# Optimization experiments

Hardware: AMD Instinct MI355X
Metric: run time of the kernel (lower is better)

## Reference

```python
import jax, jax.numpy as jnp
import numpy as np

B, T, N, P = 64, 288, 1024, 12


def setup_inputs() -> dict:
    key = jax.random.key(0)
    k1, k2 = jax.random.split(key)
    x = jax.random.normal(k1, (B, T, N, 1), dtype=jnp.float32)
    # scale AR coefficients so the self-feeding recurrence stays numerically stable
    ar_params = jax.random.normal(k2, (N, P), dtype=jnp.float32) * 0.05
    bias = jnp.zeros((N,), dtype=jnp.float32)
    return {"x": x, "ar_params": ar_params, "bias": bias}


def reference(x, ar_params, bias):
    # x: (B, T, N, 1); ar_params: (N, p); bias: (N,)
    Bd, Td, Nd, _ = x.shape
    p = ar_params.shape[1]
    # initial history window = last p entries of the full input series per (b, n)
    h0 = jnp.transpose(x[:, Td - p:, :, 0], (0, 2, 1))  # (B, N, p)

    def step(h, _):
        # per-node AR(p): dot of node coefficients with its rolling history
        pred = jnp.einsum('np,bnp->bn', ar_params, h) + bias  # (B, N)
        h = jnp.concatenate([h[:, :, 1:], pred[:, :, None]], axis=-1)
        return h, pred

    _, preds = jax.lax.scan(step, h0, None, length=Td)  # (T, B, N)
    return jnp.transpose(preds, (1, 0, 2))[..., None]  # (B, T, N, 1)
```

## Files before the change

kernel.cpp:

```cpp
#include <hip/hip_runtime.h>


constexpr int B = 64;
constexpr int T = 288;
constexpr int N = 1024;
constexpr int P = 12;
constexpr int CHUNK = 72;
constexpr int NCHUNK = T / CHUNK;

__global__ __launch_bounds__(256) void ar_chunked_kernel(
    const float* __restrict__ x,
    const float* __restrict__ ar,
    const float* __restrict__ bias,
    float* __restrict__ out)
{
    const int tid = blockIdx.x * blockDim.x + threadIdx.x;
    const int n = tid & (N - 1);
    const int b = (tid >> 10) & (B - 1);
    const int c = tid >> 16;

    float a[P];
    const float* arow = ar + n * P;
#pragma unroll
    for (int j = 0; j < P; ++j) a[j] = arow[j];
    const float bs = bias[n];

    float acc[P];
#pragma unroll
    for (int s = 0; s < P; ++s) acc[s] = bs;

    const float* xb = x + (size_t)b * T * N + (size_t)(T - P) * N + n;
#pragma unroll
    for (int i = 0; i < P; ++i) {
        const float hv = xb[(size_t)i * N];
#pragma unroll
        for (int t = 0; t <= i; ++t)
            acc[t] = fmaf(a[i - t], hv, acc[t]);
    }

    const int skip = c * CHUNK;
#pragma unroll 1
    for (int tt = 0; tt < skip; tt += P) {
#pragma unroll
        for (int k = 0; k < P; ++k) {
            const float pred = acc[k];
            acc[k] = fmaf(a[0], pred, bs);
#pragma unroll
            for (int d = 1; d < P; ++d)
                acc[(k + d) % P] = fmaf(a[P - d], pred, acc[(k + d) % P]);
        }
    }

    float* ob = out + (size_t)b * T * N + (size_t)skip * N + n;
#pragma unroll 1
    for (int tt = 0; tt < CHUNK; tt += P) {
#pragma unroll
        for (int k = 0; k < P; ++k) {
            const float pred = acc[k];
            ob[(size_t)(tt + k) * N] = pred;
            acc[k] = fmaf(a[0], pred, bs);
#pragma unroll
            for (int d = 1; d < P; ++d)
                acc[(k + d) % P] = fmaf(a[P - d], pred, acc[(k + d) % P]);
        }
    }
}

extern "C" void kernel_launch(void* const* d_in, const int* in_sizes, int n_in,
                              void* d_out, int out_size, void* d_ws, size_t ws_size,
                              hipStream_t stream) {
    const float* x    = (const float*)d_in[0];
    const float* ar   = (const float*)d_in[1];
    const float* bias = (const float*)d_in[2];
    float* out = (float*)d_out;

    const int total = B * N * NCHUNK;
    ar_chunked_kernel<<<total / 256, 256, 0, stream>>>(x, ar, bias, out);
}
```

Baseline: 126.4 us.

## Process four nodes per thread with float4 loads and stores

Each thread now runs the AR recurrence for four adjacent nodes, loading coefficients, bias, history and writing outputs as float4. The grid shrinks to one block per (batch, chunk) and the chunk count stays at four. This aims to cut memory instruction count and add instruction-level parallelism across independent recurrences. In exchange it raises register pressure and leaves far fewer waves per CU to hide latency.

```diff
diff --git a/kernel.cpp b/kernel.cpp
--- a/kernel.cpp
+++ b/kernel.cpp
@@ -5,64 +5,74 @@
 constexpr int T = 288;
 constexpr int N = 1024;
 constexpr int P = 12;
-constexpr int CHUNK = 72;
-constexpr int NCHUNK = T / CHUNK;
+constexpr int G = 4;
+constexpr int NCHUNK = 4;
+constexpr int CHUNK = T / NCHUNK;
 
-__global__ __launch_bounds__(256) void ar_chunked_kernel(
+#define STEP12(STORE_EXPR)                                                     \
+  _Pragma("unroll") for (int k = 0; k < P; ++k) {                              \
+    float pr[G];                                                               \
+    _Pragma("unroll") for (int g = 0; g < G; ++g) {                            \
+      const float pred = acc[g][k];                                            \
+      pr[g] = pred;                                                            \
+      acc[g][k] = fmaf(a[g][0], pred, bs[g]);                                  \
+      _Pragma("unroll") for (int d = 1; d < P; ++d)                            \
+        acc[g][(k + d) % P] = fmaf(a[g][P - d], pred, acc[g][(k + d) % P]);    \
+    }                                                                          \
+    STORE_EXPR;                                                                \
+  }
+
+__global__ __launch_bounds__(256) void ar_vec4_kernel(
     const float* __restrict__ x,
     const float* __restrict__ ar,
     const float* __restrict__ bias,
     float* __restrict__ out)
 {
-    const int tid = blockIdx.x * blockDim.x + threadIdx.x;
-    const int n = tid & (N - 1);
-    const int b = (tid >> 10) & (B - 1);
-    const int c = tid >> 16;
+    const int b = blockIdx.x & (B - 1);
+    const int c = blockIdx.x >> 6;
+    const int n0 = threadIdx.x * G;
 
-    float a[P];
-    const float* arow = ar + n * P;
+    float a[G][P];
 #pragma unroll
-    for (int j = 0; j < P; ++j) a[j] = arow[j];
-    const float bs = bias[n];
+    for (int g = 0; g < G; ++g) {
+        const float4* ap = (const float4*)(ar + (size_t)(n0 + g) * P);
+        const float4 a0 = ap[0], a1 = ap[1], a2 = ap[2];
+        a[g][0] = a0.x; a[g][1] = a0.y; a[g][2]  = a0.z; a[g][3]  = a0.w;
+        a[g][4] = a1.x; a[g][5] = a1.y; a[g][6]  = a1.z; a[g][7]  = a1.w;
+        a[g][8] = a2.x; a[g][9] = a2.y; a[g][10] = a2.z; a[g][11] = a2.w;
+    }
+    const float4 bv = *(const float4*)(bias + n0);
+    const float bs[G] = {bv.x, bv.y, bv.z, bv.w};
 
-    float acc[P];
+    float acc[G][P];
 #pragma unroll
-    for (int s = 0; s < P; ++s) acc[s] = bs;
+    for (int g = 0; g < G; ++g)
+#pragma unroll
+        for (int s = 0; s < P; ++s) acc[g][s] = bs[g];
 
-    const float* xb = x + (size_t)b * T * N + (size_t)(T - P) * N + n;
+    const float* xb = x + ((size_t)b * T + (T - P)) * N + n0;
 #pragma unroll
     for (int i = 0; i < P; ++i) {
-        const float hv = xb[(size_t)i * N];
+        const float4 hv = *(const float4*)(xb + (size_t)i * N);
+        const float h[G] = {hv.x, hv.y, hv.z, hv.w};
 #pragma unroll
-        for (int t = 0; t <= i; ++t)
-            acc[t] = fmaf(a[i - t], hv, acc[t]);
+        for (int g = 0; g < G; ++g)
+#pragma unroll
+            for (int t = 0; t <= i; ++t)
+                acc[g][t] = fmaf(a[g][i - t], h[g], acc[g][t]);
     }
 
     const int skip = c * CHUNK;
 #pragma unroll 1
     for (int tt = 0; tt < skip; tt += P) {
-#pragma unroll
-        for (int k = 0; k < P; ++k) {
-            const float pred = acc[k];
-            acc[k] = fmaf(a[0], pred, bs);
-#pragma unroll
-            for (int d = 1; d < P; ++d)
-                acc[(k + d) % P] = fmaf(a[P - d], pred, acc[(k + d) % P]);
-        }
+        STEP12(;)
     }
 
-    float* ob = out + (size_t)b * T * N + (size_t)skip * N + n;
+    float* ob = out + ((size_t)b * T + skip) * N + n0;
 #pragma unroll 1
     for (int tt = 0; tt < CHUNK; tt += P) {
-#pragma unroll
-        for (int k = 0; k < P; ++k) {
-            const float pred = acc[k];
-            ob[(size_t)(tt + k) * N] = pred;
-            acc[k] = fmaf(a[0], pred, bs);
-#pragma unroll
-            for (int d = 1; d < P; ++d)
-                acc[(k + d) % P] = fmaf(a[P - d], pred, acc[(k + d) % P]);
-        }
+        STEP12(*(float4*)(ob + (size_t)(tt + k) * N) =
+                   make_float4(pr[0], pr[1], pr[2], pr[3]))
     }
 }
 
@@ -74,6 +84,5 @@
     const float* bias = (const float*)d_in[2];
     float* out = (float*)d_out;
 
-    const int total = B * N * NCHUNK;
-    ar_chunked_kernel<<<total / 256, 256, 0, stream>>>(x, ar, bias, out);
+    ar_vec4_kernel<<<B * NCHUNK, 256, 0, stream>>>(x, ar, bias, out);
 }
```

Result: slower. 130.7 us (+3.4%).
